# Kernel optimization log

Measured on AMD Instinct MI355X. Metric: run time of the kernel, lower is better.

The kernel has to match this reference:

```python
import jax, jax.numpy as jnp
import numpy as np

B, NUM_RX, NUM_CHIRPS, SAMPLES = 16, 4, 64, 256
D_BINS, R_BINS = 64, 256


def _conv3d(x, w, b, pad):
    y = jax.lax.conv_general_dilated(x, w, (1, 1, 1), pad,
                                     dimension_numbers=('NCDHW', 'OIDHW', 'NCDHW'))
    return y + b[None, :, None, None, None]


def _conv2d(x, w, b, pad):
    y = jax.lax.conv_general_dilated(x, w, (1, 1), pad,
                                     dimension_numbers=('NCHW', 'OIHW', 'NCHW'))
    return y + b[None, :, None, None]


def _bn2(x, s, t):
    return x * s[None, :, None, None] + t[None, :, None, None]


def _bn3(x, s, t):
    return x * s[None, :, None, None, None] + t[None, :, None, None, None]


def _upsample_bilinear_ac(x, oh, ow):
    # torch Upsample(mode='bilinear', align_corners=True)
    _, _, h, w = x.shape
    ph = jnp.linspace(0.0, h - 1.0, oh)
    pw = jnp.linspace(0.0, w - 1.0, ow)
    h0 = jnp.clip(jnp.floor(ph).astype(jnp.int32), 0, h - 1)
    h1 = jnp.clip(h0 + 1, 0, h - 1)
    fh = ph - h0
    w0 = jnp.clip(jnp.floor(pw).astype(jnp.int32), 0, w - 1)
    w1 = jnp.clip(w0 + 1, 0, w - 1)
    fw = pw - w0
    x = x[:, :, h0, :] * (1.0 - fh)[None, None, :, None] + x[:, :, h1, :] * fh[None, None, :, None]
    x = x[:, :, :, w0] * (1.0 - fw) + x[:, :, :, w1] * fw
    return x


def setup_inputs() -> dict:
    ks = iter(jax.random.split(jax.random.key(0), 80))

    def nrm(shape, s=0.05):
        return s * jax.random.normal(next(ks), shape, dtype=jnp.float32)

    inp = {'x': jax.random.normal(next(ks), (B, NUM_RX, NUM_CHIRPS, SAMPLES, 2), dtype=jnp.float32)}

    def conv(name, shape):
        inp[name + '_w'] = nrm(shape)
        inp[name + '_b'] = nrm((shape[0],))

    def bn(name, n):  # BatchNorm in inference form folded to scale/shift
        inp[name + '_s'] = 1.0 + nrm((n,), 0.1)
        inp[name + '_t'] = nrm((n,), 0.1)

    conv('tc1', (16, 2, 1, 1, 3)); bn('tc1', 16)
    conv('tc2', (32, 16, 1, 1, 3)); bn('tc2', 32)
    conv('rx', (32, 32, NUM_RX, 1, 1)); bn('rx', 32)
    conv('cc1', (64, 32 * NUM_CHIRPS, 3, 3)); bn('cc1', 64)
    conv('cc2', (64, 64, 3, 3)); bn('cc2', 64)
    conv('rd1', (128, 64, 3, 3)); bn('rd1', 128)
    conv('rd2', (128, 128, 3, 3)); bn('rd2', 128)
    conv('up1', (64, 128, 3, 3)); bn('up1', 64)
    conv('up2', (32, 64, 3, 3)); bn('up2', 32)
    conv('up3', (1, 32, 1, 1))
    inp['wr'] = jax.random.normal(next(ks), (SAMPLES, R_BINS, 2), dtype=jnp.float32)
    inp['wd'] = jax.random.normal(next(ks), (NUM_CHIRPS, D_BINS, 2), dtype=jnp.float32)
    return inp


def reference(x, tc1_w, tc1_b, tc1_s, tc1_t, tc2_w, tc2_b, tc2_s, tc2_t,
              rx_w, rx_b, rx_s, rx_t, cc1_w, cc1_b, cc1_s, cc1_t,
              cc2_w, cc2_b, cc2_s, cc2_t, rd1_w, rd1_b, rd1_s, rd1_t,
              rd2_w, rd2_b, rd2_s, rd2_t, up1_w, up1_b, up1_s, up1_t,
              up2_w, up2_b, up2_s, up2_t, up3_w, up3_b, wr, wd):
    r = jax.nn.relu
    p3 = [(0, 0), (0, 0), (1, 1)]
    p2 = [(1, 1), (1, 1)]
    h = jnp.transpose(x, (0, 4, 1, 2, 3))                      # [B,2,RX,C,S]
    h = r(_bn3(_conv3d(h, tc1_w, tc1_b, p3), tc1_s, tc1_t))
    h = r(_bn3(_conv3d(h, tc2_w, tc2_b, p3), tc2_s, tc2_t))
    h = r(_bn3(_conv3d(h, rx_w, rx_b, [(0, 0)] * 3), rx_s, rx_t))[:, :, 0]  # [B,32,C,S]
    h = h.reshape(h.shape[0], -1, SAMPLES)[:, :, None, :]      # [B,32*C,1,S]
    h = r(_bn2(_conv2d(h, cc1_w, cc1_b, p2), cc1_s, cc1_t))
    h = r(_bn2(_conv2d(h, cc2_w, cc2_b, p2), cc2_s, cc2_t))
    h = r(_bn2(_conv2d(h, rd1_w, rd1_b, p2), rd1_s, rd1_t))
    h = r(_bn2(_conv2d(h, rd2_w, rd2_b, p2), rd2_s, rd2_t))
    h = _upsample_bilinear_ac(h, D_BINS, R_BINS)               # [B,128,D,R]
    h = r(_bn2(_conv2d(h, up1_w, up1_b, p2), up1_s, up1_t))
    h = r(_bn2(_conv2d(h, up2_w, up2_b, p2), up2_s, up2_t))
    h = jax.nn.sigmoid(_conv2d(h, up3_w, up3_b, [(0, 0), (0, 0)]))  # [B,1,D,R]
    # learnable_fft (input is real: x_imag = 0), loops -> two batched matmuls
    xr = h[:, 0]                                               # [B,D,R]
    rr = jnp.einsum('bcs,sr->bcr', xr, wr[:, :, 0])            # range DFT, real
    ri = jnp.einsum('bcs,sr->bcr', xr, wr[:, :, 1])            # range DFT, imag
    rdr = jnp.einsum('bcr,cd->bdr', rr, wd[:, :, 0]) - jnp.einsum('bcr,cd->bdr', ri, wd[:, :, 1])
    rdi = jnp.einsum('bcr,cd->bdr', rr, wd[:, :, 1]) + jnp.einsum('bcr,cd->bdr', ri, wd[:, :, 0])
    mag = jnp.sqrt(rdr * rdr + rdi * rdi) / (NUM_CHIRPS * SAMPLES)
    out = jnp.clip(h + 0.1 * mag[:, None], 0.0, 1.0)
    return jnp.transpose(out, (0, 2, 3, 1))                    # [B,D,R,1]
```

## Files before the change

kernel.cpp:

```cpp
#include <hip/hip_runtime.h>
#include <math.h>

#define OFF_A      0u
#define OFF_P      8388608u
#define OFF_WCC1   10485760u
#define OFF_BCC1   11010048u
#define OFF_WCC2   11010112u
#define OFF_BCC2   11026496u
#define OFF_WRD1   11026560u
#define OFF_BRD1   11059328u
#define OFF_WRD2   11059456u
#define OFF_BRD2   11124992u
#define OFF_WUP1   11125120u
#define OFF_BUP1   11223424u
#define OFF_WUP2   11223488u
#define OFF_BUP2   11346368u
#define OFF_WRX    11346400u
#define OFF_W1F    11350496u
#define OFF_B1F    11350592u
#define OFF_W2F    11350608u
#define OFF_B2F    11352144u
#define OFF_BRXF   11352176u
#define OFF_H      0u

__device__ __forceinline__ void fma4(float4& a, const float4& x, float w) {
  a.x = fmaf(x.x, w, a.x); a.y = fmaf(x.y, w, a.y);
  a.z = fmaf(x.z, w, a.z); a.w = fmaf(x.w, w, a.w);
}

__global__ __launch_bounds__(256) void k_repack_front(
    const float* __restrict__ tc1_w, const float* __restrict__ tc1_b, const float* __restrict__ tc1_s, const float* __restrict__ tc1_t,
    const float* __restrict__ tc2_w, const float* __restrict__ tc2_b, const float* __restrict__ tc2_s, const float* __restrict__ tc2_t,
    const float* __restrict__ rx_w, const float* __restrict__ rx_b, const float* __restrict__ rx_s, const float* __restrict__ rx_t,
    float* __restrict__ ws)
{
  const int tid = blockIdx.x * blockDim.x + threadIdx.x;
  const int nth = gridDim.x * blockDim.x;
  for (int i = tid; i < 96; i += nth) ws[OFF_W1F + i] = tc1_w[i] * tc1_s[i/6];
  for (int i = tid; i < 16; i += nth) ws[OFF_B1F + i] = tc1_b[i]*tc1_s[i] + tc1_t[i];
  for (int i = tid; i < 1536; i += nth) {
    int oc = i & 31, r = i >> 5, k = r % 3, ic = r / 3;
    ws[OFF_W2F + i] = tc2_w[oc*48 + ic*3 + k] * tc2_s[oc];
  }
  for (int i = tid; i < 32; i += nth) ws[OFF_B2F + i] = tc2_b[i]*tc2_s[i] + tc2_t[i];
  for (int i = tid; i < 4096; i += nth) {
    int oc = i & 31, ic = (i >> 5) & 31, rxi = i >> 10;
    ws[OFF_WRX + i] = rx_w[(oc*32 + ic)*4 + rxi] * rx_s[oc];
  }
  for (int i = tid; i < 32; i += nth) ws[OFF_BRXF + i] = rx_b[i]*rx_s[i] + rx_t[i];
}

__global__ __launch_bounds__(256, 4) void k_front(
    const float* __restrict__ x, const float* __restrict__ ws_c, float* __restrict__ ws,
    const float* __restrict__ cc1_w, const float* __restrict__ cc1_b, const float* __restrict__ cc1_s, const float* __restrict__ cc1_t,
    const float* __restrict__ cc2_w, const float* __restrict__ cc2_b, const float* __restrict__ cc2_s, const float* __restrict__ cc2_t,
    const float* __restrict__ rd1_w, const float* __restrict__ rd1_b, const float* __restrict__ rd1_s, const float* __restrict__ rd1_t,
    const float* __restrict__ rd2_w, const float* __restrict__ rd2_b, const float* __restrict__ rd2_s, const float* __restrict__ rd2_t,
    const float* __restrict__ up1_w, const float* __restrict__ up1_b, const float* __restrict__ up1_s, const float* __restrict__ up1_t,
    const float* __restrict__ up2_w, const float* __restrict__ up2_b, const float* __restrict__ up2_s, const float* __restrict__ up2_t,
    float* __restrict__ A)
{
  __shared__ float t1s[2][16][258];
  const int tid = threadIdx.x;

  if (blockIdx.x < 64) {
    const int t = blockIdx.x * 256 + tid;
    const int nth = 64 * 256;
    for (int i = t; i < 2048*64*4; i += nth) {
      int k = i & 3, oc = (i >> 2) & 63, c2 = i >> 8;
      ws[OFF_WCC1 + i] = (k < 3) ? cc1_w[((oc*2048 + c2)*3 + 1)*3 + k] * cc1_s[oc] : 0.f;
    }
    for (int i = t; i < 64; i += nth) ws[OFF_BCC1 + i] = cc1_b[i]*cc1_s[i] + cc1_t[i];
    for (int i = t; i < 64*64; i += nth) {
      int oc = i & 63, ic = i >> 6;
      float4 v;
      v.x = cc2_w[(oc*64 + ic)*9 + 3] * cc2_s[oc];
      v.y = cc2_w[(oc*64 + ic)*9 + 4] * cc2_s[oc];
      v.z = cc2_w[(oc*64 + ic)*9 + 5] * cc2_s[oc];
      v.w = 0.f;
      ((float4*)(ws + OFF_WCC2))[i] = v;
    }
    for (int i = t; i < 64; i += nth) ws[OFF_BCC2 + i] = cc2_b[i]*cc2_s[i] + cc2_t[i];
    for (int i = t; i < 64*128; i += nth) {
      int oc = i & 127, ic = i >> 7;
      float4 v;
      v.x = rd1_w[(oc*64 + ic)*9 + 3] * rd1_s[oc];
      v.y = rd1_w[(oc*64 + ic)*9 + 4] * rd1_s[oc];
      v.z = rd1_w[(oc*64 + ic)*9 + 5] * rd1_s[oc];
      v.w = 0.f;
      ((float4*)(ws + OFF_WRD1))[i] = v;
    }
    for (int i = t; i < 128; i += nth) ws[OFF_BRD1 + i] = rd1_b[i]*rd1_s[i] + rd1_t[i];
    for (int i = t; i < 128*128; i += nth) {
      int oc = i & 127, ic = i >> 7;
      float4 v;
      v.x = rd2_w[(oc*128 + ic)*9 + 3] * rd2_s[oc];
      v.y = rd2_w[(oc*128 + ic)*9 + 4] * rd2_s[oc];
      v.z = rd2_w[(oc*128 + ic)*9 + 5] * rd2_s[oc];
      v.w = 0.f;
      ((float4*)(ws + OFF_WRD2))[i] = v;
    }
    for (int i = t; i < 128; i += nth) ws[OFF_BRD2 + i] = rd2_b[i]*rd2_s[i] + rd2_t[i];
    for (int i = t; i < 3*128*64; i += nth) {
      int oc = i & 63, ic = (i >> 6) & 127, v = i >> 13;
      const int m = (v == 0) ? 6 : (v == 1) ? 7 : 3;
      float4 o = make_float4(0.f, 0.f, 0.f, 0.f);
      for (int kh = 0; kh < 3; ++kh)
        if ((m >> kh) & 1) {
          o.x += up1_w[((oc*128 + ic)*3 + kh)*3 + 0];
          o.y += up1_w[((oc*128 + ic)*3 + kh)*3 + 1];
          o.z += up1_w[((oc*128 + ic)*3 + kh)*3 + 2];
        }
      o.x *= up1_s[oc]; o.y *= up1_s[oc]; o.z *= up1_s[oc];
      ((float4*)(ws + OFF_WUP1))[i] = o;
    }
    for (int i = t; i < 64; i += nth) ws[OFF_BUP1 + i] = up1_b[i]*up1_s[i] + up1_t[i];
    for (int i = t; i < 5*3*64*32; i += nth) {
      int oc = i & 31, ic = (i >> 5) & 63, tt = i >> 11;
      int src = tt % 3, v = tt / 3;
      const int MASKS[15] = {2,4,0,  1,6,0,  0,7,0,  0,3,4,  0,1,2};
      const int m = MASKS[v*3 + src];
      float4 o = make_float4(0.f, 0.f, 0.f, 0.f);
      for (int kh = 0; kh < 3; ++kh)
        if ((m >> kh) & 1) {
          o.x += up2_w[((oc*64 + ic)*3 + kh)*3 + 0];
          o.y += up2_w[((oc*64 + ic)*3 + kh)*3 + 1];
          o.z += up2_w[((oc*64 + ic)*3 + kh)*3 + 2];
        }
      o.x *= up2_s[oc]; o.y *= up2_s[oc]; o.z *= up2_s[oc];
      ((float4*)(ws + OFF_WUP2))[i] = o;
    }
    for (int i = t; i < 32; i += nth) ws[OFF_BUP2 + i] = up2_b[i]*up2_s[i] + up2_t[i];
    return;
  }

  const int bb = blockIdx.x - 64;
  const int b = bb >> 6, chirp = bb & 63;
  const int s = tid;

  if (tid < 64) {
    int o = tid & 15, rr = (tid >> 4) & 1;
    int c = (tid >> 5) ? 257 : 0;
    t1s[rr][o][c] = 0.f;
  }

  const float* w1f  = ws_c + OFF_W1F;
  const float* b1f  = ws_c + OFF_B1F;
  const float* w2f  = ws_c + OFF_W2F;
  const float* b2f  = ws_c + OFF_B2F;
  const float* wrxf = ws_c + OFF_WRX;
  const float* brxf = ws_c + OFF_BRXF;

  float acc[32];
  #pragma unroll
  for (int j = 0; j < 32; ++j) acc[j] = 0.f;

  #pragma unroll 1
  for (int r2 = 0; r2 < 2; ++r2) {
    #pragma unroll
    for (int rr = 0; rr < 2; ++rr) {
      const int rxi = r2*2 + rr;
      const float2* xb2 = (const float2*)(x + ((size_t)(((b*4 + rxi)*64 + chirp)*256) << 1));
      float2 xm = xb2[s];
      float2 xl = xb2[(s == 0) ? 0 : (s - 1)];
      float2 xr = xb2[(s == 255) ? 255 : (s + 1)];
      if (s == 0)   { xl.x = 0.f; xl.y = 0.f; }
      if (s == 255) { xr.x = 0.f; xr.y = 0.f; }
      #pragma unroll 4
      for (int o = 0; o < 16; ++o) {
        const float* w = w1f + o*6;
        float v = b1f[o];
        v = fmaf(xl.x, w[0], v);
        v = fmaf(xm.x, w[1], v);
        v = fmaf(xr.x, w[2], v);
        v = fmaf(xl.y, w[3], v);
        v = fmaf(xm.y, w[4], v);
        v = fmaf(xr.y, w[5], v);
        t1s[rr][o][s+1] = fmaxf(v, 0.f);
      }
    }
    __syncthreads();

    #pragma unroll 1
    for (int rr = 0; rr < 2; ++rr) {
      const int rxi = r2*2 + rr;
      float t2[32];
      #pragma unroll
      for (int j = 0; j < 32; ++j) t2[j] = b2f[j];
      #pragma unroll 2
      for (int ic = 0; ic < 16; ++ic) {
        float tl = t1s[rr][ic][s];
        float tm = t1s[rr][ic][s+1];
        float tr = t1s[rr][ic][s+2];
        const float* w = w2f + ic*96;
        #pragma unroll
        for (int oc = 0; oc < 32; ++oc)
          t2[oc] = fmaf(tl, w[oc], fmaf(tm, w[32+oc], fmaf(tr, w[64+oc], t2[oc])));
      }
      #pragma unroll
      for (int j = 0; j < 32; ++j) t2[j] = fmaxf(t2[j], 0.f);

      const float* wr0 = wrxf + rxi*1024;
      #pragma unroll 4
      for (int ic = 0; ic < 32; ++ic) {
        float tv = t2[ic];
        const float* w = wr0 + ic*32;
        #pragma unroll
        for (int oc = 0; oc < 32; ++oc)
          acc[oc] = fmaf(tv, w[oc], acc[oc]);
      }
    }
    __syncthreads();
  }

  #pragma unroll 4
  for (int oc = 0; oc < 32; ++oc) {
    float v = fmaxf(acc[oc] + brxf[oc], 0.f);
    A[(size_t)((b*2048 + oc*64 + chirp)*256) + s] = v;
  }
}

__global__ __launch_bounds__(256) void k_cc1(
    const float* __restrict__ A, const float* __restrict__ wp, float* __restrict__ P)
{
  __shared__ __align__(16) float As[256][36];
  const int tid = threadIdx.x;
  const int ks = blockIdx.x & 7;
  const int stile = (blockIdx.x >> 3) & 7;
  const int b = blockIdx.x >> 6;
  const int s0 = stile * 32;
  const int oc = tid & 63;
  const int sg = tid >> 6;
  const int cbase = ks * 256;
  const float4* w4 = (const float4*)wp;

  for (int i = tid; i < 256*36; i += 256) {
    int c = i / 36, si = i - c*36;
    int sA = s0 - 1 + si;
    float v = 0.f;
    if (si < 34 && sA >= 0 && sA < 256)
      v = A[(size_t)(b*2048 + cbase + c)*256 + sA];
    As[c][si] = v;
  }
  __syncthreads();

  const int sb = sg * 8;
  float4 acc0 = make_float4(0.f,0.f,0.f,0.f);
  float4 acc1 = make_float4(0.f,0.f,0.f,0.f);
  #pragma unroll 4
  for (int c = 0; c < 256; ++c) {
    float4 w = w4[(size_t)(cbase + c)*64 + oc];
    float4 a0 = *(const float4*)&As[c][sb];
    float4 a1 = *(const float4*)&As[c][sb + 4];
    float2 a2 = *(const float2*)&As[c][sb + 8];
    acc0.x = fmaf(a0.x,w.x, fmaf(a0.y,w.y, fmaf(a0.z,w.z, acc0.x)));
    acc0.y = fmaf(a0.y,w.x, fmaf(a0.z,w.y, fmaf(a0.w,w.z, acc0.y)));
    acc0.z = fmaf(a0.z,w.x, fmaf(a0.w,w.y, fmaf(a1.x,w.z, acc0.z)));
    acc0.w = fmaf(a0.w,w.x, fmaf(a1.x,w.y, fmaf(a1.y,w.z, acc0.w)));
    acc1.x = fmaf(a1.x,w.x, fmaf(a1.y,w.y, fmaf(a1.z,w.z, acc1.x)));
    acc1.y = fmaf(a1.y,w.x, fmaf(a1.z,w.y, fmaf(a1.w,w.z, acc1.y)));
    acc1.z = fmaf(a1.z,w.x, fmaf(a1.w,w.y, fmaf(a2.x,w.z, acc1.z)));
    acc1.w = fmaf(a1.w,w.x, fmaf(a2.x,w.y, fmaf(a2.y,w.z, acc1.w)));
  }
  float* Pk = P + ((size_t)(ks*16 + b)*256)*64;
  int s = s0 + sb;
  Pk[(size_t)(s+0)*64 + oc] = acc0.x;
  Pk[(size_t)(s+1)*64 + oc] = acc0.y;
  Pk[(size_t)(s+2)*64 + oc] = acc0.z;
  Pk[(size_t)(s+3)*64 + oc] = acc0.w;
  Pk[(size_t)(s+4)*64 + oc] = acc1.x;
  Pk[(size_t)(s+5)*64 + oc] = acc1.y;
  Pk[(size_t)(s+6)*64 + oc] = acc1.z;
  Pk[(size_t)(s+7)*64 + oc] = acc1.w;
}

__global__ __launch_bounds__(256) void k_midup(
    const float* __restrict__ P, const float* __restrict__ bcc1,
    const float* __restrict__ wcc2, const float* __restrict__ bcc2,
    const float* __restrict__ wrd1, const float* __restrict__ brd1,
    const float* __restrict__ wrd2, const float* __restrict__ brd2,
    const float* __restrict__ wup1, const float* __restrict__ bup1,
    const float* __restrict__ wup2, const float* __restrict__ bup2,
    const float* __restrict__ up3_w, const float* __restrict__ up3_b,
    float* __restrict__ H)
{
  __shared__ __align__(16) float bufA[2560];
  __shared__ __align__(16) float bufB[2560];
  __shared__ float u2s[5][32][9];
  float* c1s = bufA;
  float* c2s = bufA + 1280;
  float* r1s = bufB;
  float* Rls = bufA;
  float* u1s = bufB;

  const int tid = threadIdx.x;
  const int b = blockIdx.x >> 5;
  const int s0 = (blockIdx.x & 31) * 8;
  const float4* wc2 = (const float4*)wcc2;
  const float4* wr1 = (const float4*)wrd1;
  const float4* wr2 = (const float4*)wrd2;
  const float4* wu1 = (const float4*)wup1;
  const float4* wu2 = (const float4*)wup2;

  for (int i = tid; i < 18*64; i += 256) {
    int ic = i & 63, si = i >> 6;
    int sA = s0 - 5 + si;
    float v = 0.f;
    if (sA >= 0 && sA < 256) {
      float a = bcc1[ic];
      #pragma unroll
      for (int ksp = 0; ksp < 8; ++ksp)
        a += P[((size_t)(ksp*16 + b)*256 + sA)*64 + ic];
      v = fmaxf(a, 0.f);
    }
    c1s[ic*20 + si] = v;
  }
  __syncthreads();

  {
    const int g = tid >> 6, oc = tid & 63;
    float bb = bcc2[oc];
    float4 acc = make_float4(bb, bb, bb, bb);
    #pragma unroll 4
    for (int ic = 0; ic < 64; ++ic) {
      float4 w = wc2[ic*64 + oc];
      float4 ca = *(const float4*)&c1s[ic*20 + g*4];
      float2 cb = *(const float2*)&c1s[ic*20 + g*4 + 4];
      acc.x = fmaf(ca.x,w.x, fmaf(ca.y,w.y, fmaf(ca.z,w.z, acc.x)));
      acc.y = fmaf(ca.y,w.x, fmaf(ca.z,w.y, fmaf(ca.w,w.z, acc.y)));
      acc.z = fmaf(ca.z,w.x, fmaf(ca.w,w.y, fmaf(cb.x,w.z, acc.z)));
      acc.w = fmaf(ca.w,w.x, fmaf(cb.x,w.y, fmaf(cb.y,w.z, acc.w)));
    }
    float r[4] = {acc.x, acc.y, acc.z, acc.w};
    #pragma unroll
    for (int j = 0; j < 4; ++j) {
      int si = g*4 + j, sA = s0 - 4 + si;
      c2s[oc*20 + si] = (sA >= 0 && sA < 256) ? fmaxf(r[j], 0.f) : 0.f;
    }
    c2s[oc*20 + 16 + g] = 0.f;
  }
  __syncthreads();

  {
    const int oc = tid & 127, g = tid >> 7;
    float bb = brd1[oc];
    float a[8];
    #pragma unroll
    for (int j = 0; j < 8; ++j) a[j] = bb;
    #pragma unroll 4
    for (int ic = 0; ic < 64; ++ic) {
      float4 w = wr1[ic*128 + oc];
      float4 ca = *(const float4*)&c2s[ic*20 + g*8];
      float4 cb = *(const float4*)&c2s[ic*20 + g*8 + 4];
      float2 cc = *(const float2*)&c2s[ic*20 + g*8 + 8];
      float r[10] = {ca.x,ca.y,ca.z,ca.w, cb.x,cb.y,cb.z,cb.w, cc.x,cc.y};
      #pragma unroll
      for (int j = 0; j < 8; ++j)
        a[j] = fmaf(r[j],w.x, fmaf(r[j+1],w.y, fmaf(r[j+2],w.z, a[j])));
    }
    #pragma unroll
    for (int j = 0; j < 8; ++j) {
      int si = g*8 + j, sA = s0 - 3 + si;
      if (si < 14)
        r1s[oc*20 + si] = (sA >= 0 && sA < 256) ? fmaxf(a[j], 0.f) : 0.f;
    }
  }
  #pragma unroll
  for (int k = 0; k < 3; ++k) {
    int idx = k*256 + tid;
    int ic = idx & 127, si = 14 + (idx >> 7);
    r1s[ic*20 + si] = 0.f;
  }
  __syncthreads();

  {
    const int oc = tid & 127, g = tid >> 7;
    float bb = brd2[oc];
    float a[8];
    #pragma unroll
    for (int j = 0; j < 8; ++j) a[j] = bb;
    #pragma unroll 4
    for (int ic = 0; ic < 128; ++ic) {
      float4 w = wr2[ic*128 + oc];
      float4 ca = *(const float4*)&r1s[ic*20 + g*8];
      float4 cb = *(const float4*)&r1s[ic*20 + g*8 + 4];
      float2 cc = *(const float2*)&r1s[ic*20 + g*8 + 8];
      float r[10] = {ca.x,ca.y,ca.z,ca.w, cb.x,cb.y,cb.z,cb.w, cc.x,cc.y};
      #pragma unroll
      for (int j = 0; j < 8; ++j)
        a[j] = fmaf(r[j],w.x, fmaf(r[j+1],w.y, fmaf(r[j+2],w.z, a[j])));
    }
    __syncthreads();
    #pragma unroll
    for (int j = 0; j < 8; ++j) {
      int si = g*8 + j, sA = s0 - 2 + si;
      if (si < 12)
        Rls[oc*12 + si] = (sA >= 0 && sA < 256) ? fmaxf(a[j], 0.f) : 0.f;
    }
  }
  __syncthreads();

  {
    float a[10];
    const int vi = tid >> 6, oc = tid & 63;
    if (vi < 3) {
      float bb = bup1[oc];
      #pragma unroll
      for (int p = 0; p < 10; ++p) a[p] = bb;
      #pragma unroll 4
      for (int ic = 0; ic < 128; ++ic) {
        float4 w = wu1[(vi*128 + ic)*64 + oc];
        float4 ra = *(const float4*)&Rls[ic*12 + 0];
        float4 rb = *(const float4*)&Rls[ic*12 + 4];
        float4 rc = *(const float4*)&Rls[ic*12 + 8];
        float r[12] = {ra.x,ra.y,ra.z,ra.w, rb.x,rb.y,rb.z,rb.w, rc.x,rc.y,rc.z,rc.w};
        #pragma unroll
        for (int p = 0; p < 10; ++p)
          a[p] = fmaf(r[p],w.x, fmaf(r[p+1],w.y, fmaf(r[p+2],w.z, a[p])));
      }
    }
    __syncthreads();
    if (vi < 3) {
      #pragma unroll
      for (int p = 0; p < 10; ++p) {
        int sA = s0 - 1 + p;
        u1s[(vi*64 + oc)*12 + p] = (sA >= 0 && sA < 256) ? fmaxf(a[p], 0.f) : 0.f;
      }
      u1s[(vi*64 + oc)*12 + 10] = 0.f;
      u1s[(vi*64 + oc)*12 + 11] = 0.f;
    }
  }
  __syncthreads();

  if (tid < 160) {
    const int v = tid >> 5, oc = tid & 31;
    float a[8];
    float bb = bup2[oc];
    #pragma unroll
    for (int p = 0; p < 8; ++p) a[p] = bb;
    for (int src = 0; src < 3; ++src) {
      #pragma unroll 4
      for (int ic = 0; ic < 64; ++ic) {
        float4 w = wu2[((v*3 + src)*64 + ic)*32 + oc];
        float4 ua = *(const float4*)&u1s[(src*64 + ic)*12 + 0];
        float4 ub = *(const float4*)&u1s[(src*64 + ic)*12 + 4];
        float2 uc = *(const float2*)&u1s[(src*64 + ic)*12 + 8];
        float r[10] = {ua.x,ua.y,ua.z,ua.w, ub.x,ub.y,ub.z,ub.w, uc.x,uc.y};
        #pragma unroll
        for (int p = 0; p < 8; ++p)
          a[p] = fmaf(r[p],w.x, fmaf(r[p+1],w.y, fmaf(r[p+2],w.z, a[p])));
      }
    }
    #pragma unroll
    for (int p = 0; p < 8; ++p) u2s[v][oc][p] = fmaxf(a[p], 0.f);
  }
  __syncthreads();

  if (tid < 40) {
    int v = tid >> 3, j = tid & 7;
    float a = up3_b[0];
    for (int ic = 0; ic < 32; ++ic)
      a = fmaf(u2s[v][ic][j], up3_w[ic], a);
    H[(size_t)(b*5 + v)*256 + s0 + j] = 1.f / (1.f + expf(-a));
  }
}

__global__ __launch_bounds__(256) void k_spec(
    const float* __restrict__ H, const float* __restrict__ wr, const float* __restrict__ wd,
    float* __restrict__ out)
{
  __shared__ float hs[5][256];
  __shared__ float S0[64], S1[64];
  __shared__ float wds[4][64][2];
  __shared__ float ps[16][16][10];
  __shared__ float rred[16][10];
  const int tid = threadIdx.x;
  const int b = blockIdx.x >> 4;
  const int rt = blockIdx.x & 15;
  const int r0 = rt * 16;

  for (int i = tid; i < 1280; i += 256) hs[i >> 8][i & 255] = H[(size_t)b*1280 + i];
  if (tid < 64) {
    const float2* wd2 = (const float2*)wd;
    float a0 = 0.f, a1 = 0.f;
    for (int c = 2; c <= 61; ++c) {
      float2 v = wd2[c*64 + tid];
      a0 += v.x; a1 += v.y;
    }
    S0[tid] = a0; S1[tid] = a1;
  }
  for (int i = tid; i < 512; i += 256) {
    int row = i >> 7, rem = i & 127, d = rem >> 1, comp = rem & 1;
    int c = (row < 2) ? row : (60 + row);
    wds[row][d][comp] = wd[(c*64 + d)*2 + comp];
  }
  __syncthreads();

  {
    const int rl = tid & 15;
    const int sq = tid >> 4;
    const int r = r0 + rl;
    float rr[5] = {0,0,0,0,0}, ri[5] = {0,0,0,0,0};
    const float2* wr2p = (const float2*)wr;
    for (int s = sq*16; s < sq*16 + 16; ++s) {
      float2 w = wr2p[s*256 + r];
      #pragma unroll
      for (int k = 0; k < 5; ++k) {
        float hv = hs[k][s];
        rr[k] = fmaf(hv, w.x, rr[k]);
        ri[k] = fmaf(hv, w.y, ri[k]);
      }
    }
    #pragma unroll
    for (int k = 0; k < 5; ++k) {
      ps[sq][rl][k]     = rr[k];
      ps[sq][rl][5 + k] = ri[k];
    }
  }
  __syncthreads();

  if (tid < 160) {
    const int rl = tid & 15, k = tid >> 4;
    float a = 0.f;
    #pragma unroll
    for (int sq = 0; sq < 16; ++sq) a += ps[sq][rl][k];
    rred[rl][k] = a;
  }
  __syncthreads();

  {
    const int rl = tid & 15, dg = tid >> 4;
    const int r = r0 + rl;
    float Rr[5], Ri[5];
    #pragma unroll
    for (int k = 0; k < 5; ++k) { Rr[k] = rred[rl][k]; Ri[k] = rred[rl][5 + k]; }
    for (int dd = 0; dd < 4; ++dd) {
      int d = dg*4 + dd;
      float w0r = wds[0][d][0], w0i = wds[0][d][1];
      float w1r = wds[1][d][0], w1i = wds[1][d][1];
      float w2r = wds[2][d][0], w2i = wds[2][d][1];
      float w3r = wds[3][d][0], w3i = wds[3][d][1];
      float s0v = S0[d], s1v = S1[d];
      float rdr = Rr[0]*w0r + Rr[1]*w1r + Rr[2]*s0v + Rr[3]*w2r + Rr[4]*w3r
                - Ri[0]*w0i - Ri[1]*w1i - Ri[2]*s1v - Ri[3]*w2i - Ri[4]*w3i;
      float rdi = Rr[0]*w0i + Rr[1]*w1i + Rr[2]*s1v + Rr[3]*w2i + Rr[4]*w3i
                + Ri[0]*w0r + Ri[1]*w1r + Ri[2]*s0v + Ri[3]*w2r + Ri[4]*w3r;
      float mag = sqrtf(rdr*rdr + rdi*rdi) * (1.0f / 16384.0f);
      int v = (d == 0) ? 0 : (d == 1) ? 1 : (d <= 61) ? 2 : ((d == 62) ? 3 : 4);
      float o = hs[v][r] + 0.1f * mag;
      out[(size_t)b*16384 + d*256 + r] = fminf(fmaxf(o, 0.f), 1.f);
    }
  }
}

extern "C" void kernel_launch(void* const* d_in, const int* in_sizes, int n_in,
                              void* d_out, int out_size, void* d_ws, size_t ws_size,
                              hipStream_t stream)
{
  const float* x     = (const float*)d_in[0];
  const float* tc1_w = (const float*)d_in[1];  const float* tc1_b = (const float*)d_in[2];
  const float* tc1_s = (const float*)d_in[3];  const float* tc1_t = (const float*)d_in[4];
  const float* tc2_w = (const float*)d_in[5];  const float* tc2_b = (const float*)d_in[6];
  const float* tc2_s = (const float*)d_in[7];  const float* tc2_t = (const float*)d_in[8];
  const float* rx_w  = (const float*)d_in[9];  const float* rx_b  = (const float*)d_in[10];
  const float* rx_s  = (const float*)d_in[11]; const float* rx_t  = (const float*)d_in[12];
  const float* cc1_w = (const float*)d_in[13]; const float* cc1_b = (const float*)d_in[14];
  const float* cc1_s = (const float*)d_in[15]; const float* cc1_t = (const float*)d_in[16];
  const float* cc2_w = (const float*)d_in[17]; const float* cc2_b = (const float*)d_in[18];
  const float* cc2_s = (const float*)d_in[19]; const float* cc2_t = (const float*)d_in[20];
  const float* rd1_w = (const float*)d_in[21]; const float* rd1_b = (const float*)d_in[22];
  const float* rd1_s = (const float*)d_in[23]; const float* rd1_t = (const float*)d_in[24];
  const float* rd2_w = (const float*)d_in[25]; const float* rd2_b = (const float*)d_in[26];
  const float* rd2_s = (const float*)d_in[27]; const float* rd2_t = (const float*)d_in[28];
  const float* up1_w = (const float*)d_in[29]; const float* up1_b = (const float*)d_in[30];
  const float* up1_s = (const float*)d_in[31]; const float* up1_t = (const float*)d_in[32];
  const float* up2_w = (const float*)d_in[33]; const float* up2_b = (const float*)d_in[34];
  const float* up2_s = (const float*)d_in[35]; const float* up2_t = (const float*)d_in[36];
  const float* up3_w = (const float*)d_in[37]; const float* up3_b = (const float*)d_in[38];
  const float* wr    = (const float*)d_in[39];
  const float* wd    = (const float*)d_in[40];
  float* ws  = (float*)d_ws;
  float* out = (float*)d_out;

  k_repack_front<<<8, 256, 0, stream>>>(tc1_w, tc1_b, tc1_s, tc1_t,
                                        tc2_w, tc2_b, tc2_s, tc2_t,
                                        rx_w, rx_b, rx_s, rx_t, ws);
  k_front<<<1088, 256, 0, stream>>>(x, ws, ws,
                                    cc1_w, cc1_b, cc1_s, cc1_t,
                                    cc2_w, cc2_b, cc2_s, cc2_t,
                                    rd1_w, rd1_b, rd1_s, rd1_t,
                                    rd2_w, rd2_b, rd2_s, rd2_t,
                                    up1_w, up1_b, up1_s, up1_t,
                                    up2_w, up2_b, up2_s, up2_t,
                                    ws + OFF_A);
  k_cc1<<<1024, 256, 0, stream>>>(ws + OFF_A, ws + OFF_WCC1, ws + OFF_P);
  k_midup<<<512, 256, 0, stream>>>(ws + OFF_P, ws + OFF_BCC1,
                                   ws + OFF_WCC2, ws + OFF_BCC2,
                                   ws + OFF_WRD1, ws + OFF_BRD1,
                                   ws + OFF_WRD2, ws + OFF_BRD2,
                                   ws + OFF_WUP1, ws + OFF_BUP1,
                                   ws + OFF_WUP2, ws + OFF_BUP2,
                                   up3_w, up3_b, ws + OFF_H);
  k_spec<<<256, 256, 0, stream>>>(ws + OFF_H, wr, wd, out);
}
```

Measured before the change: 357.6 us.

## Remap rd/up conv threads to fewer warps with more outputs each

The front kernel's time-conv stage now processes one rx channel per iteration with a single shared buffer instead of pairs, which shrinks shared memory and may allow higher occupancy. In the decoder tail, rd1/rd2 use 128 threads each computing two output channels, dropping the redundant padded positions. up1 and up2 use fewer threads, with each thread reusing loaded activations across 3 kernel rows or 5 output rows. This cuts redundant LDS reads and wasted padding work, but it serialises more work per thread and leaves half the block idle.

Measured after the change: 418.0 us. +16.9%, slower.

```diff
diff --git a/kernel.cpp b/kernel.cpp
--- a/kernel.cpp
+++ b/kernel.cpp
@@ -60,7 +60,7 @@
     const float* __restrict__ up2_w, const float* __restrict__ up2_b, const float* __restrict__ up2_s, const float* __restrict__ up2_t,
     float* __restrict__ A)
 {
-  __shared__ float t1s[2][16][258];
+  __shared__ float t1s[16][258];
   const int tid = threadIdx.x;
 
   if (blockIdx.x < 64) {
@@ -138,11 +138,7 @@
   const int b = bb >> 6, chirp = bb & 63;
   const int s = tid;
 
-  if (tid < 64) {
-    int o = tid & 15, rr = (tid >> 4) & 1;
-    int c = (tid >> 5) ? 257 : 0;
-    t1s[rr][o][c] = 0.f;
-  }
+  if (tid < 32) { int o = tid & 15; int c = (tid >> 4) ? 257 : 0; t1s[o][c] = 0.f; }
 
   const float* w1f  = ws_c + OFF_W1F;
   const float* b1f  = ws_c + OFF_B1F;
@@ -156,10 +152,8 @@
   for (int j = 0; j < 32; ++j) acc[j] = 0.f;
 
   #pragma unroll 1
-  for (int r2 = 0; r2 < 2; ++r2) {
-    #pragma unroll
-    for (int rr = 0; rr < 2; ++rr) {
-      const int rxi = r2*2 + rr;
+  for (int rxi = 0; rxi < 4; ++rxi) {
+    {
       const float2* xb2 = (const float2*)(x + ((size_t)(((b*4 + rxi)*64 + chirp)*256) << 1));
       float2 xm = xb2[s];
       float2 xl = xb2[(s == 0) ? 0 : (s - 1)];
@@ -176,39 +170,35 @@
         v = fmaf(xl.y, w[3], v);
         v = fmaf(xm.y, w[4], v);
         v = fmaf(xr.y, w[5], v);
-        t1s[rr][o][s+1] = fmaxf(v, 0.f);
+        t1s[o][s+1] = fmaxf(v, 0.f);
       }
     }
     __syncthreads();
 
-    #pragma unroll 1
-    for (int rr = 0; rr < 2; ++rr) {
-      const int rxi = r2*2 + rr;
-      float t2[32];
-      #pragma unroll
-      for (int j = 0; j < 32; ++j) t2[j] = b2f[j];
-      #pragma unroll 2
-      for (int ic = 0; ic < 16; ++ic) {
-        float tl = t1s[rr][ic][s];
-        float tm = t1s[rr][ic][s+1];
-        float tr = t1s[rr][ic][s+2];
-        const float* w = w2f + ic*96;
-        #pragma unroll
-        for (int oc = 0; oc < 32; ++oc)
-          t2[oc] = fmaf(tl, w[oc], fmaf(tm, w[32+oc], fmaf(tr, w[64+oc], t2[oc])));
-      }
-      #pragma unroll
-      for (int j = 0; j < 32; ++j) t2[j] = fmaxf(t2[j], 0.f);
-
-      const float* wr0 = wrxf + rxi*1024;
-      #pragma unroll 4
-      for (int ic = 0; ic < 32; ++ic) {
-        float tv = t2[ic];
-        const float* w = wr0 + ic*32;
-        #pragma unroll
-        for (int oc = 0; oc < 32; ++oc)
-          acc[oc] = fmaf(tv, w[oc], acc[oc]);
-      }
+    float t2[32];
+    #pragma unroll
+    for (int j = 0; j < 32; ++j) t2[j] = b2f[j];
+    #pragma unroll 2
+    for (int ic = 0; ic < 16; ++ic) {
+      float tl = t1s[ic][s];
+      float tm = t1s[ic][s+1];
+      float tr = t1s[ic][s+2];
+      const float* w = w2f + ic*96;
+      #pragma unroll
+      for (int oc = 0; oc < 32; ++oc)
+        t2[oc] = fmaf(tl, w[oc], fmaf(tm, w[32+oc], fmaf(tr, w[64+oc], t2[oc])));
+    }
+    #pragma unroll
+    for (int j = 0; j < 32; ++j) t2[j] = fmaxf(t2[j], 0.f);
+
+    const float* wr0 = wrxf + rxi*1024;
+    #pragma unroll 4
+    for (int ic = 0; ic < 32; ++ic) {
+      float tv = t2[ic];
+      const float* w = wr0 + ic*32;
+      #pragma unroll
+      for (int oc = 0; oc < 32; ++oc)
+        acc[oc] = fmaf(tv, w[oc], acc[oc]);
     }
     __syncthreads();
   }
@@ -341,28 +331,36 @@
   }
   __syncthreads();
 
-  {
-    const int oc = tid & 127, g = tid >> 7;
-    float bb = brd1[oc];
-    float a[8];
-    #pragma unroll
-    for (int j = 0; j < 8; ++j) a[j] = bb;
+  if (tid < 128) {
+    const int ocp = tid & 63, g = tid >> 6;
+    const int oc0 = ocp*2, oc1 = oc0 + 1;
+    const int p0 = g * 8;
+    const int np = g ? 6 : 8;
+    float bb0 = brd1[oc0], bb1 = brd1[oc1];
+    float a0[8], a1[8];
+    #pragma unroll
+    for (int j = 0; j < 8; ++j) { a0[j] = bb0; a1[j] = bb1; }
     #pragma unroll 4
     for (int ic = 0; ic < 64; ++ic) {
-      float4 w = wr1[ic*128 + oc];
-      float4 ca = *(const float4*)&c2s[ic*20 + g*8];
-      float4 cb = *(const float4*)&c2s[ic*20 + g*8 + 4];
-      float2 cc = *(const float2*)&c2s[ic*20 + g*8 + 8];
-      float r[10] = {ca.x,ca.y,ca.z,ca.w, cb.x,cb.y,cb.z,cb.w, cc.x,cc.y};
-      #pragma unroll
-      for (int j = 0; j < 8; ++j)
-        a[j] = fmaf(r[j],w.x, fmaf(r[j+1],w.y, fmaf(r[j+2],w.z, a[j])));
-    }
-    #pragma unroll
-    for (int j = 0; j < 8; ++j) {
-      int si = g*8 + j, sA = s0 - 3 + si;
-      if (si < 14)
-        r1s[oc*20 + si] = (sA >= 0 && sA < 256) ? fmaxf(a[j], 0.f) : 0.f;
+      float4 w0 = wr1[ic*128 + oc0];
+      float4 w1 = wr1[ic*128 + oc1];
+      const float* base = &c2s[ic*20 + p0];
+      float4 ra = *(const float4*)base;
+      float4 rb = *(const float4*)(base + 4);
+      float2 rc = *(const float2*)(base + 8);
+      float r[10] = {ra.x,ra.y,ra.z,ra.w, rb.x,rb.y,rb.z,rb.w, rc.x,rc.y};
+      #pragma unroll
+      for (int j = 0; j < 8; ++j) {
+        a0[j] = fmaf(r[j],w0.x, fmaf(r[j+1],w0.y, fmaf(r[j+2],w0.z, a0[j])));
+        a1[j] = fmaf(r[j],w1.x, fmaf(r[j+1],w1.y, fmaf(r[j+2],w1.z, a1[j])));
+      }
+    }
+    for (int j = 0; j < np; ++j) {
+      int si = p0 + j, sA = s0 - 3 + si;
+      float m0 = (sA >= 0 && sA < 256) ? fmaxf(a0[j], 0.f) : 0.f;
+      float m1 = (sA >= 0 && sA < 256) ? fmaxf(a1[j], 0.f) : 0.f;
+      r1s[oc0*20 + si] = m0;
+      r1s[oc1*20 + si] = m1;
     }
   }
   #pragma unroll
@@ -373,86 +371,121 @@
   }
   __syncthreads();
 
-  {
-    const int oc = tid & 127, g = tid >> 7;
-    float bb = brd2[oc];
-    float a[8];
-    #pragma unroll
-    for (int j = 0; j < 8; ++j) a[j] = bb;
+  if (tid < 128) {
+    const int ocp = tid & 63, g = tid >> 6;
+    const int oc0 = ocp*2, oc1 = oc0 + 1;
+    const int p0 = g * 8;
+    const int np = g ? 4 : 8;
+    float bb0 = brd2[oc0], bb1 = brd2[oc1];
+    float a0[8], a1[8];
+    #pragma unroll
+    for (int j = 0; j < 8; ++j) { a0[j] = bb0; a1[j] = bb1; }
     #pragma unroll 4
     for (int ic = 0; ic < 128; ++ic) {
-      float4 w = wr2[ic*128 + oc];
-      float4 ca = *(const float4*)&r1s[ic*20 + g*8];
-      float4 cb = *(const float4*)&r1s[ic*20 + g*8 + 4];
-      float2 cc = *(const float2*)&r1s[ic*20 + g*8 + 8];
-      float r[10] = {ca.x,ca.y,ca.z,ca.w, cb.x,cb.y,cb.z,cb.w, cc.x,cc.y};
-      #pragma unroll
-      for (int j = 0; j < 8; ++j)
-        a[j] = fmaf(r[j],w.x, fmaf(r[j+1],w.y, fmaf(r[j+2],w.z, a[j])));
+      float4 w0 = wr2[ic*128 + oc0];
+      float4 w1 = wr2[ic*128 + oc1];
+      const float* base = &r1s[ic*20 + p0];
+      float4 ra = *(const float4*)base;
+      float4 rb = *(const float4*)(base + 4);
+      float2 rc = *(const float2*)(base + 8);
+      float r[10] = {ra.x,ra.y,ra.z,ra.w, rb.x,rb.y,rb.z,rb.w, rc.x,rc.y};
+      #pragma unroll
+      for (int j = 0; j < 8; ++j) {
+        a0[j] = fmaf(r[j],w0.x, fmaf(r[j+1],w0.y, fmaf(r[j+2],w0.z, a0[j])));
+        a1[j] = fmaf(r[j],w1.x, fmaf(r[j+1],w1.y, fmaf(r[j+2],w1.z, a1[j])));
+      }
     }
     __syncthreads();
-    #pragma unroll
-    for (int j = 0; j < 8; ++j) {
-      int si = g*8 + j, sA = s0 - 2 + si;
-      if (si < 12)
-        Rls[oc*12 + si] = (sA >= 0 && sA < 256) ? fmaxf(a[j], 0.f) : 0.f;
-    }
+    for (int j = 0; j < np; ++j) {
+      int si = p0 + j, sA = s0 - 2 + si;
+      float m0 = (sA >= 0 && sA < 256) ? fmaxf(a0[j], 0.f) : 0.f;
+      float m1 = (sA >= 0 && sA < 256) ? fmaxf(a1[j], 0.f) : 0.f;
+      Rls[oc0*12 + si] = m0;
+      Rls[oc1*12 + si] = m1;
+    }
+  } else {
+    __syncthreads();
   }
   __syncthreads();
 
   {
-    float a[10];
-    const int vi = tid >> 6, oc = tid & 63;
-    if (vi < 3) {
-      float bb = bup1[oc];
-      #pragma unroll
-      for (int p = 0; p < 10; ++p) a[p] = bb;
-      #pragma unroll 4
+    const int oc = tid & 63, g = (tid >> 6) & 1;
+    const int active = (tid < 128);
+    const int p0 = g * 5;
+    const int lo = g * 4;
+    float bb = active ? bup1[oc] : 0.f;
+    float a0[5], a1[5], a2v[5];
+    #pragma unroll
+    for (int j = 0; j < 5; ++j) { a0[j] = bb; a1[j] = bb; a2v[j] = bb; }
+    if (active) {
+      #pragma unroll 2
       for (int ic = 0; ic < 128; ++ic) {
-        float4 w = wu1[(vi*128 + ic)*64 + oc];
-        float4 ra = *(const float4*)&Rls[ic*12 + 0];
-        float4 rb = *(const float4*)&Rls[ic*12 + 4];
-        float4 rc = *(const float4*)&Rls[ic*12 + 8];
-        float r[12] = {ra.x,ra.y,ra.z,ra.w, rb.x,rb.y,rb.z,rb.w, rc.x,rc.y,rc.z,rc.w};
+        float4 w0 = wu1[(0*128 + ic)*64 + oc];
+        float4 w1 = wu1[(1*128 + ic)*64 + oc];
+        float4 w2 = wu1[(2*128 + ic)*64 + oc];
+        const float* base = &Rls[ic*12 + lo];
+        float4 ra = *(const float4*)base;
+        float4 rb = *(const float4*)(base + 4);
+        float r[8] = {ra.x,ra.y,ra.z,ra.w, rb.x,rb.y,rb.z,rb.w};
+        const int off = g;
         #pragma unroll
-        for (int p = 0; p < 10; ++p)
-          a[p] = fmaf(r[p],w.x, fmaf(r[p+1],w.y, fmaf(r[p+2],w.z, a[p])));
+        for (int j = 0; j < 5; ++j) {
+          float x0 = r[j+off], x1 = r[j+off+1], x2 = r[j+off+2];
+          a0[j]  = fmaf(x0,w0.x, fmaf(x1,w0.y, fmaf(x2,w0.z, a0[j])));
+          a1[j]  = fmaf(x0,w1.x, fmaf(x1,w1.y, fmaf(x2,w1.z, a1[j])));
+          a2v[j] = fmaf(x0,w2.x, fmaf(x1,w2.y, fmaf(x2,w2.z, a2v[j])));
+        }
       }
     }
     __syncthreads();
-    if (vi < 3) {
-      #pragma unroll
-      for (int p = 0; p < 10; ++p) {
-        int sA = s0 - 1 + p;
-        u1s[(vi*64 + oc)*12 + p] = (sA >= 0 && sA < 256) ? fmaxf(a[p], 0.f) : 0.f;
-      }
-      u1s[(vi*64 + oc)*12 + 10] = 0.f;
-      u1s[(vi*64 + oc)*12 + 11] = 0.f;
-    }
-  }
-  __syncthreads();
-
-  if (tid < 160) {
-    const int v = tid >> 5, oc = tid & 31;
-    float a[8];
+    if (active) {
+      #pragma unroll
+      for (int j = 0; j < 5; ++j) {
+        int p = p0 + j, sA = s0 - 1 + p;
+        int ok = (sA >= 0 && sA < 256);
+        u1s[(0*64 + oc)*12 + p] = ok ? fmaxf(a0[j], 0.f) : 0.f;
+        u1s[(1*64 + oc)*12 + p] = ok ? fmaxf(a1[j], 0.f) : 0.f;
+        u1s[(2*64 + oc)*12 + p] = ok ? fmaxf(a2v[j], 0.f) : 0.f;
+      }
+      if (g) {
+        u1s[(0*64 + oc)*12 + 10] = 0.f; u1s[(0*64 + oc)*12 + 11] = 0.f;
+        u1s[(1*64 + oc)*12 + 10] = 0.f; u1s[(1*64 + oc)*12 + 11] = 0.f;
+        u1s[(2*64 + oc)*12 + 10] = 0.f; u1s[(2*64 + oc)*12 + 11] = 0.f;
+      }
+    }
+  }
+  __syncthreads();
+
+  if (tid < 64) {
+    const int oc = tid & 31, g = tid >> 5;
+    const int p0 = g * 4;
     float bb = bup2[oc];
-    #pragma unroll
-    for (int p = 0; p < 8; ++p) a[p] = bb;
+    float a[5][4];
+    #pragma unroll
+    for (int v = 0; v < 5; ++v)
+      #pragma unroll
+      for (int j = 0; j < 4; ++j) a[v][j] = bb;
     for (int src = 0; src < 3; ++src) {
-      #pragma unroll 4
+      #pragma unroll 2
       for (int ic = 0; ic < 64; ++ic) {
-        float4 w = wu2[((v*3 + src)*64 + ic)*32 + oc];
-        float4 ua = *(const float4*)&u1s[(src*64 + ic)*12 + 0];
-        float4 ub = *(const float4*)&u1s[(src*64 + ic)*12 + 4];
-        float2 uc = *(const float2*)&u1s[(src*64 + ic)*12 + 8];
-        float r[10] = {ua.x,ua.y,ua.z,ua.w, ub.x,ub.y,ub.z,ub.w, uc.x,uc.y};
+        const float* base = &u1s[(src*64 + ic)*12 + p0];
+        float4 ua = *(const float4*)base;
+        float2 ub = *(const float2*)(base + 4);
+        float r[6] = {ua.x,ua.y,ua.z,ua.w, ub.x,ub.y};
         #pragma unroll
-        for (int p = 0; p < 8; ++p)
-          a[p] = fmaf(r[p],w.x, fmaf(r[p+1],w.y, fmaf(r[p+2],w.z, a[p])));
-      }
-    }
-    #pragma unroll
-    for (int p = 0; p < 8; ++p) u2s[v][oc][p] = fmaxf(a[p], 0.f);
+        for (int v = 0; v < 5; ++v) {
+          float4 w = wu2[((v*3 + src)*64 + ic)*32 + oc];
+          #pragma unroll
+          for (int j = 0; j < 4; ++j)
+            a[v][j] = fmaf(r[j],w.x, fmaf(r[j+1],w.y, fmaf(r[j+2],w.z, a[v][j])));
+        }
+      }
+    }
+    #pragma unroll
+    for (int v = 0; v < 5; ++v)
+      #pragma unroll
+      for (int j = 0; j < 4; ++j)
+        u2s[v][oc][p0 + j] = fmaxf(a[v][j], 0.f);
   }
   __syncthreads();
 
```
